# Kernel tuning notes

Hardware: AMD Instinct MI355X
Metric: run time of the kernel (lower is better)

The kernel has to match this reference:

```python
import jax, jax.numpy as jnp
import numpy as np

D_MODEL = 256
N_BINS = 11
# standard KNRM kernels: exact-match bin (mu=1, sigma=1e-3) + 10 soft bins
MUS = jnp.array([1.0, 0.9, 0.7, 0.5, 0.3, 0.1, -0.1, -0.3, -0.5, -0.7, -0.9], dtype=jnp.float32)
SIGMAS = jnp.array([1e-3] + [0.1] * 10, dtype=jnp.float32)


def _l2norm(x, eps=1e-10):
    # F.normalize(p=2, eps=1e-10): x / max(||x||, eps)
    n = jnp.sqrt(jnp.sum(x * x, axis=-1, keepdims=True))
    return x / jnp.maximum(n, eps)


def setup_inputs() -> dict:
    key = jax.random.key(0)
    ks = jax.random.split(key, 10)
    B, NB, Q, T, D = 64, 8, 32, 256, D_MODEL
    return {
        "word_atten": jax.random.uniform(ks[0], (B, NB, Q), dtype=jnp.float32),
        "hq": jax.random.normal(ks[1], (B, NB, Q, D), dtype=jnp.float32),
        "can": jax.random.normal(ks[2], (B, T, D), dtype=jnp.float32),
        "rep": jax.random.normal(ks[3], (B, NB, D), dtype=jnp.float32),
        "rep_cur": jax.random.normal(ks[4], (B, D), dtype=jnp.float32),
        "mask_hq": jnp.ones((B, NB, Q), dtype=jnp.float32),
        "mask_can": jnp.ones((B, T), dtype=jnp.float32),
        "mask_session": jnp.ones((B, NB), dtype=jnp.float32),
        "W_dense": jax.random.normal(ks[5], (N_BINS, 1), dtype=jnp.float32) * 0.3,
        "b_dense": jnp.zeros((1,), dtype=jnp.float32),
        "W_att": jax.random.normal(ks[6], (D, D), dtype=jnp.float32) * (1.0 / np.sqrt(D)),
        "b_att": jnp.zeros((D,), dtype=jnp.float32),
    }


def reference(word_atten, hq, can, rep, rep_cur, mask_hq, mask_can, mask_session,
              W_dense, b_dense, W_att, b_att):
    # cosine-similarity matrix: [B, NB, Q, T]
    hq_n = _l2norm(hq)
    can_n = _l2norm(can)
    matrix = jnp.einsum("bnqd,btd->bnqt", hq_n, can_n)

    # Gaussian kernel soft-binning: expand to [B, NB, Q, T, N_BINS]
    diff = matrix[..., None] - MUS  # broadcast over bins
    kern = jnp.exp(-(diff * diff) / (2.0 * SIGMAS * SIGMAS))
    kern = kern * mask_can[:, None, None, :, None]  # mask doc tokens
    pooling_sum = jnp.sum(kern, axis=3)  # [B, NB, Q, N_BINS]

    log_pool = jnp.log(jnp.clip(pooling_sum, 1e-10)) * 0.01
    log_pool = log_pool * mask_hq[..., None] * word_atten[..., None]
    pooled = jnp.sum(log_pool, axis=2)  # [B, NB, N_BINS]

    pooled = pooled * mask_session[..., None]

    # attention over session blocks (AttendAttention): scaled dot with projected current rep
    q = rep_cur @ W_att + b_att  # [B, D]
    scores = jnp.einsum("bnd,bd->bn", rep, q) / np.sqrt(D_MODEL).astype(np.float32)
    scores = jnp.where(mask_session > 0, scores, -1e9)
    attn = jax.nn.softmax(scores, axis=-1)  # [B, NB]

    score = jnp.tanh(pooled @ W_dense + b_dense).squeeze(-1)  # [B, NB]
    return jnp.sum(score * attn, axis=1)  # [B]
```

## Files before the change

### kernel.cpp

```cpp
#include <hip/hip_runtime.h>

#define B_ 64
#define NB_ 8
#define Q_ 32
#define T_ 256
#define D_ 256
#define NBINS 11

typedef __attribute__((ext_vector_type(8))) short bf16x8;
typedef __attribute__((ext_vector_type(4))) float f32x4;
typedef unsigned short ushort_t;
typedef unsigned int uint_t;

#define CANH_OFF 0u
#define CANL_OFF 8388608u
#define HQH_OFF 16777216u
#define HQL_OFF 25165824u
#define PSUM_OFF 33554432u

__device__ inline ushort_t bf16_rnd(float f) {
  uint_t u = __float_as_uint(f);
  return (ushort_t)((u + 0x8000u) >> 16);
}
__device__ inline uint_t pack2(ushort_t a, ushort_t b) {
  return (uint_t)a | ((uint_t)b << 16);
}

__device__ inline void bins_acc(f32x4 acc, float mk, float binacc[4][NBINS]) {
  const float mus[NBINS] = {1.0f, 0.9f, 0.7f, 0.5f, 0.3f, 0.1f,
                            -0.1f, -0.3f, -0.5f, -0.7f, -0.9f};
  const float nis2[NBINS] = {-5.0e5f, -50.f, -50.f, -50.f, -50.f, -50.f,
                             -50.f, -50.f, -50.f, -50.f, -50.f};
#pragma unroll
  for (int r = 0; r < 4; r++) {
    float v0 = acc[r];
#pragma unroll
    for (int j = 0; j < NBINS; j++) {
      float d0 = v0 - mus[j];
      binacc[r][j] += mk * __expf(d0 * d0 * nis2[j]);
    }
  }
}

__global__ __launch_bounds__(256) void split_kernel(
    const float* __restrict__ can, const float* __restrict__ hq,
    uint4* __restrict__ canH, uint4* __restrict__ canL,
    uint4* __restrict__ hqH, uint4* __restrict__ hqL) {
  __shared__ __align__(16) ushort_t sm_hi[32 * 264];
  __shared__ __align__(16) ushort_t sm_lo[32 * 264];
  int blk = blockIdx.x;
  int tid = threadIdx.x;
  const float* src;
  uint4 *dH, *dL;
  int tilebase;
  if (blk < 512) {
    int b = blk >> 3, ch = blk & 7;
    src = can + ((size_t)b * T_ + ch * 32) * D_;
    dH = canH;
    dL = canL;
    tilebase = b * 16 + ch * 2;
  } else {
    int outb = blk - 512;
    src = hq + (size_t)outb * (Q_ * D_);
    dH = hqH;
    dL = hqL;
    tilebase = outb * 2;
  }

#pragma unroll
  for (int it = 0; it < 4; it++) {
    int flat = it * 2048 + tid * 8;
    int row = flat >> 8, col = flat & 255;
    const float* p = src + row * D_ + col;
    float4 x = reinterpret_cast<const float4*>(p)[0];
    float4 y = reinterpret_cast<const float4*>(p)[1];
    float s = x.x * x.x + x.y * x.y + x.z * x.z + x.w * x.w +
              y.x * y.x + y.y * y.y + y.z * y.z + y.w * y.w;
    s += __shfl_xor(s, 1);
    s += __shfl_xor(s, 2);
    s += __shfl_xor(s, 4);
    s += __shfl_xor(s, 8);
    s += __shfl_xor(s, 16);
    float inv = 1.0f / fmaxf(sqrtf(s), 1e-10f);
    float v[8] = {x.x, x.y, x.z, x.w, y.x, y.y, y.z, y.w};
    ushort_t h[8], l[8];
#pragma unroll
    for (int j = 0; j < 8; j++) {
      float sv = v[j] * inv;
      h[j] = bf16_rnd(sv);
      float hf = __uint_as_float(((uint_t)h[j]) << 16);
      l[j] = bf16_rnd(sv - hf);
    }
    uint4 ph = {pack2(h[0], h[1]), pack2(h[2], h[3]), pack2(h[4], h[5]),
                pack2(h[6], h[7])};
    uint4 pl = {pack2(l[0], l[1]), pack2(l[2], l[3]), pack2(l[4], l[5]),
                pack2(l[6], l[7])};
    *reinterpret_cast<uint4*>(&sm_hi[row * 264 + col]) = ph;
    *reinterpret_cast<uint4*>(&sm_lo[row * 264 + col]) = pl;
  }
  __syncthreads();
  int wv = tid >> 6, lane = tid & 63;
  int tl = wv >> 1, part = wv & 1;
  int lq = lane & 15, lk = lane >> 4;
  const ushort_t* smp = part ? sm_lo : sm_hi;
  uint4* dst = part ? dL : dH;
#pragma unroll
  for (int kk = 0; kk < 8; kk++) {
    const ushort_t* a = &smp[(tl * 16 + lq) * 264 + kk * 32 + lk * 8];
    dst[((size_t)(tilebase + tl) * 8 + kk) * 64 + lane] =
        *reinterpret_cast<const uint4*>(a);
  }
}

__global__ __launch_bounds__(256, 2) void pool_kernel(
    const uint4* __restrict__ hqH, const uint4* __restrict__ hqL,
    const uint4* __restrict__ canH, const uint4* __restrict__ canL,
    const float* __restrict__ mask_can, float* __restrict__ psum) {
  __shared__ float partial[4 * 16 * NBINS];

  int i = blockIdx.x;
  int b = i & 63;
  int rest = i >> 6;
  int nb = rest & 7, ts = rest >> 3;
  int outb = b * NB_ + nb;
  int tid = threadIdx.x;
  int wv = tid >> 6, lane = tid & 63;
  int lq = lane & 15, lk = lane >> 4;
  int mtile = wv & 1, tq = wv >> 1;

  bf16x8 ah[8], al[8];
  size_t abase = (size_t)(outb * 2 + mtile) * 512 + lane;
#pragma unroll
  for (int kk = 0; kk < 8; kk++) {
    ah[kk] = *reinterpret_cast<const bf16x8*>(&hqH[abase + kk * 64]);
    al[kk] = *reinterpret_cast<const bf16x8*>(&hqL[abase + kk * 64]);
  }

  int t0 = ts * 4 + tq * 2;
  float mk0 = mask_can[b * T_ + (t0 + 0) * 16 + lq];
  float mk1 = mask_can[b * T_ + (t0 + 1) * 16 + lq];

  float binacc[4][NBINS];
#pragma unroll
  for (int r = 0; r < 4; r++)
#pragma unroll
    for (int j = 0; j < NBINS; j++) binacc[r][j] = 0.0f;

  size_t bbase = (size_t)(b * 16 + t0) * 512 + lane;
  f32x4 acc0 = {0.f, 0.f, 0.f, 0.f};
#pragma unroll
  for (int kk = 0; kk < 8; kk++) {
    bf16x8 bh = *reinterpret_cast<const bf16x8*>(&canH[bbase + kk * 64]);
    bf16x8 bl = *reinterpret_cast<const bf16x8*>(&canL[bbase + kk * 64]);
    acc0 = __builtin_amdgcn_mfma_f32_16x16x32_bf16(ah[kk], bh, acc0, 0, 0, 0);
    acc0 = __builtin_amdgcn_mfma_f32_16x16x32_bf16(al[kk], bh, acc0, 0, 0, 0);
    acc0 = __builtin_amdgcn_mfma_f32_16x16x32_bf16(ah[kk], bl, acc0, 0, 0, 0);
  }
  bf16x8 bh1[8], bl1[8];
#pragma unroll
  for (int kk = 0; kk < 8; kk++) {
    bh1[kk] = *reinterpret_cast<const bf16x8*>(&canH[bbase + 512 + kk * 64]);
    bl1[kk] = *reinterpret_cast<const bf16x8*>(&canL[bbase + 512 + kk * 64]);
  }
  bins_acc(acc0, mk0, binacc);
  f32x4 acc1 = {0.f, 0.f, 0.f, 0.f};
#pragma unroll
  for (int kk = 0; kk < 8; kk++) {
    acc1 = __builtin_amdgcn_mfma_f32_16x16x32_bf16(ah[kk], bh1[kk], acc1, 0, 0, 0);
    acc1 = __builtin_amdgcn_mfma_f32_16x16x32_bf16(al[kk], bh1[kk], acc1, 0, 0, 0);
    acc1 = __builtin_amdgcn_mfma_f32_16x16x32_bf16(ah[kk], bl1[kk], acc1, 0, 0, 0);
  }
  bins_acc(acc1, mk1, binacc);

#pragma unroll
  for (int r = 0; r < 4; r++)
#pragma unroll
    for (int j = 0; j < NBINS; j++) {
      float v = binacc[r][j];
      v += __shfl_xor(v, 1);
      v += __shfl_xor(v, 2);
      v += __shfl_xor(v, 4);
      v += __shfl_xor(v, 8);
      binacc[r][j] = v;
    }
  if (lq == 0) {
#pragma unroll
    for (int r = 0; r < 4; r++)
#pragma unroll
      for (int j = 0; j < NBINS; j++)
        partial[(wv * 16 + lk * 4 + r) * NBINS + j] = binacc[r][j];
  }
  __syncthreads();

  for (int idx = tid; idx < Q_ * NBINS; idx += 256) {
    int q = idx / NBINS;
    int j = idx - q * NBINS;
    int m = q >> 4, r16 = q & 15;
    float s = partial[((0 + m) * 16 + r16) * NBINS + j] +
              partial[((2 + m) * 16 + r16) * NBINS + j];
    psum[((size_t)(outb * 4 + ts)) * (Q_ * NBINS) + idx] = s;
  }
}

__global__ __launch_bounds__(256) void finish_kernel(
    const float* __restrict__ psum, const float* __restrict__ word_atten,
    const float* __restrict__ mask_hq, const float* __restrict__ rep,
    const float* __restrict__ rep_cur, const float* __restrict__ mask_session,
    const float* __restrict__ W_dense, const float* __restrict__ b_dense,
    const float* __restrict__ W_att, const float* __restrict__ b_att,
    float* __restrict__ out) {
  __shared__ float qproj[256];
  __shared__ float lp_sm[NB_ * Q_ * NBINS];
  __shared__ float pooled_sm[NB_ * NBINS];
  __shared__ float scores_sm[NB_];

  int b = blockIdx.x;
  int tid = threadIdx.x;
  int wv = tid >> 6, lane = tid & 63;

  if (wv < 2) {
    const float* rc = rep_cur + b * D_;
    float a0 = b_att[tid], a1 = b_att[tid + 128];
#pragma unroll 8
    for (int k = 0; k < D_; k++) {
      float r = rc[k];
      a0 += r * W_att[k * D_ + tid];
      a1 += r * W_att[k * D_ + tid + 128];
    }
    qproj[tid] = a0;
    qproj[tid + 128] = a1;
  } else {
    int t2 = tid - 128;
    for (int idx = t2; idx < NB_ * Q_ * NBINS; idx += 128) {
      int nn = idx / (Q_ * NBINS);
      int rem = idx - nn * (Q_ * NBINS);
      int q = rem / NBINS;
      int outb = b * NB_ + nn;
      const float* pp = psum + ((size_t)outb * 4) * (Q_ * NBINS) + rem;
      float s = pp[0] + pp[Q_ * NBINS] + pp[2 * Q_ * NBINS] +
                pp[3 * Q_ * NBINS];
      float wa = word_atten[outb * Q_ + q] * mask_hq[outb * Q_ + q];
      lp_sm[idx] = logf(fmaxf(s, 1e-10f)) * 0.01f * wa;
    }
  }
  __syncthreads();

  if (tid < NB_ * NBINS) {
    int nn = tid / NBINS, j = tid - nn * NBINS;
    float s = 0.f;
#pragma unroll
    for (int q = 0; q < Q_; q++) s += lp_sm[(nn * Q_ + q) * NBINS + j];
    pooled_sm[tid] = s;
  }

  for (int nn = wv; nn < NB_; nn += 4) {
    const float* rp = rep + ((size_t)b * NB_ + nn) * D_;
    float4 r4 = reinterpret_cast<const float4*>(rp)[lane];
    float4 q4 = *reinterpret_cast<float4*>(&qproj[lane * 4]);
    float s = r4.x * q4.x + r4.y * q4.y + r4.z * q4.z + r4.w * q4.w;
#pragma unroll
    for (int off = 32; off > 0; off >>= 1) s += __shfl_down(s, off);
    if (lane == 0) scores_sm[nn] = s * 0.0625f;
  }
  __syncthreads();

  if (tid == 0) {
    float sc[NB_];
    float mx = -1e30f;
    for (int nn = 0; nn < NB_; nn++) {
      float s = (mask_session[b * NB_ + nn] > 0.f) ? scores_sm[nn] : -1e9f;
      sc[nn] = s;
      mx = fmaxf(mx, s);
    }
    float den = 0.f;
    for (int nn = 0; nn < NB_; nn++) {
      sc[nn] = __expf(sc[nn] - mx);
      den += sc[nn];
    }
    float invd = 1.0f / den;
    float res = 0.f;
    for (int nn = 0; nn < NB_; nn++) {
      float ms = mask_session[b * NB_ + nn];
      float pw = b_dense[0];
#pragma unroll
      for (int j = 0; j < NBINS; j++)
        pw += pooled_sm[nn * NBINS + j] * ms * W_dense[j];
      res += tanhf(pw) * sc[nn] * invd;
    }
    out[b] = res;
  }
}

extern "C" void kernel_launch(void* const* d_in, const int* in_sizes, int n_in,
                              void* d_out, int out_size, void* d_ws,
                              size_t ws_size, hipStream_t stream) {
  const float* word_atten = (const float*)d_in[0];
  const float* hq = (const float*)d_in[1];
  const float* can = (const float*)d_in[2];
  const float* rep = (const float*)d_in[3];
  const float* rep_cur = (const float*)d_in[4];
  const float* mask_hq = (const float*)d_in[5];
  const float* mask_can = (const float*)d_in[6];
  const float* mask_session = (const float*)d_in[7];
  const float* W_dense = (const float*)d_in[8];
  const float* b_dense = (const float*)d_in[9];
  const float* W_att = (const float*)d_in[10];
  const float* b_att = (const float*)d_in[11];
  float* out = (float*)d_out;

  char* ws = (char*)d_ws;
  uint4* canH = (uint4*)(ws + CANH_OFF);
  uint4* canL = (uint4*)(ws + CANL_OFF);
  uint4* hqH = (uint4*)(ws + HQH_OFF);
  uint4* hqL = (uint4*)(ws + HQL_OFF);
  float* psum = (float*)(ws + PSUM_OFF);

  hipLaunchKernelGGL(split_kernel, dim3(1024), dim3(256), 0, stream, can, hq,
                     canH, canL, hqH, hqL);
  hipLaunchKernelGGL(pool_kernel, dim3(2048), dim3(256), 0, stream, hqH, hqL,
                     canH, canL, mask_can, psum);
  hipLaunchKernelGGL(finish_kernel, dim3(B_), dim3(256), 0, stream, psum,
                     word_atten, mask_hq, rep, rep_cur, mask_session, W_dense,
                     b_dense, W_att, b_att, out);
}
```

Before: 139.7 us.

## Cover all doc tiles per block with double-buffered LDS staging of candidate tiles

The pool kernel now handles all 256 document tokens per (batch, block) instead of splitting T across four blocks, which cuts the grid from 2048 to 512 blocks. Candidate hi/lo tiles are staged into a double-buffered LDS area and shared between the two M-tile waves. The global load of the next tile overlaps the MFMAs and bin accumulation of the current one. This removes the partial-sum reduction in the finish kernel and the duplicate candidate loads per wave. In exchange it adds LDS use (64 KB), a barrier per tile and lower parallelism, so fewer waves are available to hide latency.

```diff
diff --git a/kernel.cpp b/kernel.cpp
--- a/kernel.cpp
+++ b/kernel.cpp
@@ -116,12 +116,12 @@
     const uint4* __restrict__ hqH, const uint4* __restrict__ hqL,
     const uint4* __restrict__ canH, const uint4* __restrict__ canL,
     const float* __restrict__ mask_can, float* __restrict__ psum) {
+  __shared__ __align__(16) ushort_t ldsB[2][2][2][4096];
   __shared__ float partial[4 * 16 * NBINS];
 
   int i = blockIdx.x;
   int b = i & 63;
-  int rest = i >> 6;
-  int nb = rest & 7, ts = rest >> 3;
+  int nb = i >> 6;
   int outb = b * NB_ + nb;
   int tid = threadIdx.x;
   int wv = tid >> 6, lane = tid & 63;
@@ -136,9 +136,27 @@
     al[kk] = *reinterpret_cast<const bf16x8*>(&hqL[abase + kk * 64]);
   }
 
-  int t0 = ts * 4 + tq * 2;
-  float mk0 = mask_can[b * T_ + (t0 + 0) * 16 + lq];
-  float mk1 = mask_can[b * T_ + (t0 + 1) * 16 + lq];
+  float mkv[8];
+#pragma unroll
+  for (int ti = 0; ti < 8; ti++)
+    mkv[ti] = mask_can[b * T_ + (tq * 8 + ti) * 16 + lq];
+
+  const uint4* srcP = mtile ? canL : canH;
+  ushort_t* sb = &ldsB[tq][0][0][0];
+  const int BUFSTRIDE = 2 * 4096;
+  int myPart = mtile * 4096;
+
+  size_t tbase = (size_t)(b * 16 + tq * 8) * 512 + lane;
+
+  {
+    uint4 stg[8];
+#pragma unroll
+    for (int kk = 0; kk < 8; kk++) stg[kk] = srcP[tbase + kk * 64];
+#pragma unroll
+    for (int kk = 0; kk < 8; kk++)
+      *reinterpret_cast<uint4*>(&sb[myPart + kk * 512 + lane * 8]) = stg[kk];
+  }
+  __syncthreads();
 
   float binacc[4][NBINS];
 #pragma unroll
@@ -146,31 +164,42 @@
 #pragma unroll
     for (int j = 0; j < NBINS; j++) binacc[r][j] = 0.0f;
 
-  size_t bbase = (size_t)(b * 16 + t0) * 512 + lane;
-  f32x4 acc0 = {0.f, 0.f, 0.f, 0.f};
-#pragma unroll
-  for (int kk = 0; kk < 8; kk++) {
-    bf16x8 bh = *reinterpret_cast<const bf16x8*>(&canH[bbase + kk * 64]);
-    bf16x8 bl = *reinterpret_cast<const bf16x8*>(&canL[bbase + kk * 64]);
-    acc0 = __builtin_amdgcn_mfma_f32_16x16x32_bf16(ah[kk], bh, acc0, 0, 0, 0);
-    acc0 = __builtin_amdgcn_mfma_f32_16x16x32_bf16(al[kk], bh, acc0, 0, 0, 0);
-    acc0 = __builtin_amdgcn_mfma_f32_16x16x32_bf16(ah[kk], bl, acc0, 0, 0, 0);
-  }
-  bf16x8 bh1[8], bl1[8];
-#pragma unroll
-  for (int kk = 0; kk < 8; kk++) {
-    bh1[kk] = *reinterpret_cast<const bf16x8*>(&canH[bbase + 512 + kk * 64]);
-    bl1[kk] = *reinterpret_cast<const bf16x8*>(&canL[bbase + 512 + kk * 64]);
-  }
-  bins_acc(acc0, mk0, binacc);
-  f32x4 acc1 = {0.f, 0.f, 0.f, 0.f};
-#pragma unroll
-  for (int kk = 0; kk < 8; kk++) {
-    acc1 = __builtin_amdgcn_mfma_f32_16x16x32_bf16(ah[kk], bh1[kk], acc1, 0, 0, 0);
-    acc1 = __builtin_amdgcn_mfma_f32_16x16x32_bf16(al[kk], bh1[kk], acc1, 0, 0, 0);
-    acc1 = __builtin_amdgcn_mfma_f32_16x16x32_bf16(ah[kk], bl1[kk], acc1, 0, 0, 0);
-  }
-  bins_acc(acc1, mk1, binacc);
+  f32x4 accPrev;
+  float mkPrev = 0.0f;
+  int bufoff = 0;
+
+  for (int ti = 0; ti < 8; ti++) {
+    uint4 stg[8];
+    if (ti < 7) {
+#pragma unroll
+      for (int kk = 0; kk < 8; kk++)
+        stg[kk] = srcP[tbase + (size_t)(ti + 1) * 512 + kk * 64];
+    }
+    f32x4 acc = {0.f, 0.f, 0.f, 0.f};
+#pragma unroll
+    for (int kk = 0; kk < 8; kk++) {
+      bf16x8 bh = *reinterpret_cast<const bf16x8*>(
+          &sb[bufoff + 0 + kk * 512 + lane * 8]);
+      bf16x8 bl = *reinterpret_cast<const bf16x8*>(
+          &sb[bufoff + 4096 + kk * 512 + lane * 8]);
+      acc = __builtin_amdgcn_mfma_f32_16x16x32_bf16(ah[kk], bh, acc, 0, 0, 0);
+      acc = __builtin_amdgcn_mfma_f32_16x16x32_bf16(al[kk], bh, acc, 0, 0, 0);
+      acc = __builtin_amdgcn_mfma_f32_16x16x32_bf16(ah[kk], bl, acc, 0, 0, 0);
+    }
+    if (ti > 0) bins_acc(accPrev, mkPrev, binacc);
+    accPrev = acc;
+    mkPrev = mkv[ti];
+    if (ti < 7) {
+      int ob = bufoff ^ BUFSTRIDE;
+#pragma unroll
+      for (int kk = 0; kk < 8; kk++)
+        *reinterpret_cast<uint4*>(&sb[ob + myPart + kk * 512 + lane * 8]) =
+            stg[kk];
+    }
+    __syncthreads();
+    bufoff ^= BUFSTRIDE;
+  }
+  bins_acc(accPrev, mkPrev, binacc);
 
 #pragma unroll
   for (int r = 0; r < 4; r++)
@@ -198,7 +227,7 @@
     int m = q >> 4, r16 = q & 15;
     float s = partial[((0 + m) * 16 + r16) * NBINS + j] +
               partial[((2 + m) * 16 + r16) * NBINS + j];
-    psum[((size_t)(outb * 4 + ts)) * (Q_ * NBINS) + idx] = s;
+    psum[(size_t)outb * (Q_ * NBINS) + idx] = s;
   }
 }
 
@@ -236,9 +265,7 @@
       int rem = idx - nn * (Q_ * NBINS);
       int q = rem / NBINS;
       int outb = b * NB_ + nn;
-      const float* pp = psum + ((size_t)outb * 4) * (Q_ * NBINS) + rem;
-      float s = pp[0] + pp[Q_ * NBINS] + pp[2 * Q_ * NBINS] +
-                pp[3 * Q_ * NBINS];
+      float s = psum[(size_t)outb * (Q_ * NBINS) + rem];
       float wa = word_atten[outb * Q_ + q] * mask_hq[outb * Q_ + q];
       lp_sm[idx] = logf(fmaxf(s, 1e-10f)) * 0.01f * wa;
     }
@@ -317,7 +344,7 @@
 
   hipLaunchKernelGGL(split_kernel, dim3(1024), dim3(256), 0, stream, can, hq,
                      canH, canL, hqH, hqL);
-  hipLaunchKernelGGL(pool_kernel, dim3(2048), dim3(256), 0, stream, hqH, hqL,
+  hipLaunchKernelGGL(pool_kernel, dim3(512), dim3(256), 0, stream, hqH, hqL,
                      canH, canL, mask_can, psum);
   hipLaunchKernelGGL(finish_kernel, dim3(B_), dim3(256), 0, stream, psum,
                      word_atten, mask_hq, rep, rep_cur, mask_session, W_dense,
```

Result: slower. 169.9 us (+21.6%).
